# Kernel tuning notes

Hardware: AMD Instinct MI355X
Metric: run time of the kernel (lower is better)

## Reference

```python
import jax, jax.numpy as jnp
import numpy as np

# Module hyperparameters derived from init_kwargs
G = 100          # grid_size = int(n_samples ** gamma) = int(10000 ** 0.5)
K = 3            # KAN_SPLINE_ORDER
NB = G + K       # num_basis = 103
H = (1.5 - (-0.5)) / G
# grid identical for every input feature (torch expands a 1D grid)
GRID = jnp.arange(-K, G + K + 1, dtype=jnp.float32) * H - 0.5  # (G + 2K + 1,)


def bspline_basis(x):
    """Cox-de Boor recursion. x: (B, F) -> (B, F, NB)."""
    g = GRID
    xe = x[..., None]  # (B, F, 1)
    bases = ((xe >= g[:-1]) & (xe < g[1:])).astype(x.dtype)  # (B, F, G+2K)
    for k in range(1, K + 1):
        left = (xe - g[:-(k + 1)]) / jnp.maximum(g[k:-1] - g[:-(k + 1)], 1e-8)
        right = (g[k + 1:] - xe) / jnp.maximum(g[k + 1:] - g[1:-k], 1e-8)
        bases = left * bases[..., :-1] + right * bases[..., 1:]
    return bases  # (B, F, NB)


def kan_layer(x, bw, sw, wb, ws, residual):
    # base path: SiLU activation then linear
    base_out = jax.nn.silu(x) @ bw.T                      # (B, out)
    # spline path: basis expansion then contraction with spline_weight
    spline_out = jnp.einsum('bin,oin->bo', bspline_basis(x), sw)
    out = wb * base_out + ws * spline_out
    return out + x if residual else out


def setup_inputs() -> dict:
    key = jax.random.key(0)
    ks = jax.random.split(key, 16)
    B, D, W = 2048, 64, 243
    inp = {'x': jax.random.uniform(ks[0], (B, D), dtype=jnp.float32)}
    dims = [(D, W), (W, W), (W, W), (W, W), (W, W), (W, 1)]
    for i, (fi, fo) in enumerate(dims):
        kb, ksw = jax.random.split(jax.random.fold_in(key, i + 1))
        inp[f'bw{i}'] = jax.random.normal(kb, (fo, fi), dtype=jnp.float32) * (1.0 / np.sqrt(fi))
        # torch init: uniform(-0.5/G, 0.5/G)
        inp[f'sw{i}'] = jax.random.uniform(ksw, (fo, fi, NB), dtype=jnp.float32,
                                           minval=-0.5 / G, maxval=0.5 / G)
        inp[f'wb{i}'] = jnp.zeros((1,), dtype=jnp.float32)
        inp[f'ws{i}'] = jnp.ones((1,), dtype=jnp.float32)
    return inp


def reference(x, bw0, sw0, wb0, ws0, bw1, sw1, wb1, ws1, bw2, sw2, wb2, ws2,
              bw3, sw3, wb3, ws3, bw4, sw4, wb4, ws4, bw5, sw5, wb5, ws5):
    layers = [
        (bw0, sw0, wb0, ws0, False),  # 64 -> 243 (in != out: no residual)
        (bw1, sw1, wb1, ws1, True),
        (bw2, sw2, wb2, ws2, True),
        (bw3, sw3, wb3, ws3, True),
        (bw4, sw4, wb4, ws4, True),
        (bw5, sw5, wb5, ws5, False),  # 243 -> 1 (use_residual=False)
    ]
    h = x
    for bw, sw, wb, ws, res in layers:
        h = kan_layer(h, bw, sw, wb, ws, res)
    return h
```

## Files before the change

kernel.cpp:

```cpp
#include <hip/hip_runtime.h>
#include <hip/hip_fp16.h>
#include <math.h>

#define BATCH 2048
#define NBAS 103
#define NPAIR 102
#define OUTR 243
#define OUTP 256

typedef _Float16 half2v __attribute__((ext_vector_type(2)));

__device__ __forceinline__ float dot2(unsigned a, unsigned b, float c) {
#if __has_builtin(__builtin_amdgcn_fdot2)
    return __builtin_amdgcn_fdot2(__builtin_bit_cast(half2v, a),
                                  __builtin_bit_cast(half2v, b), c, false);
#else
    __half2 ha = __builtin_bit_cast(__half2, a), hb = __builtin_bit_cast(__half2, b);
    c = fmaf(__low2float(ha), __low2float(hb), c);
    c = fmaf(__high2float(ha), __high2float(hb), c);
    return c;
#endif
}

__device__ __forceinline__ uint4 make_meta(float x, int i) {
    float u = (x + 0.56f) * 50.0f;
    bool inr = (u >= 0.0f) && (u < 106.0f);
    float fj = floorf(u);
    float t = u - fj;
    int j = (int)fj;
    j = j < -1 ? -1 : (j > 106 ? 106 : j);
    float omt = 1.0f - t;
    float t2 = t * t, t3 = t2 * t;
    float w[4];
    w[0] = omt * omt * omt * (1.0f / 6.0f);
    w[1] = (3.0f * t3 - 6.0f * t2 + 4.0f) * (1.0f / 6.0f);
    w[2] = (-3.0f * t3 + 3.0f * t2 + 3.0f * t + 1.0f) * (1.0f / 6.0f);
    w[3] = t3 * (1.0f / 6.0f);
    int idx = j - 3;
    int idxc = idx < 0 ? 0 : (idx > 99 ? 99 : idx);
    int d = idx - idxc;
    float wc[4];
    #pragma unroll
    for (int m = 0; m < 4; ++m) {
        int s = m - d;
        wc[m] = (inr && s >= 0 && s < 4) ? w[s] : 0.0f;
    }
    __half2 w01 = __floats2half2_rn(wc[0], wc[1]);
    __half2 w23 = __floats2half2_rn(wc[2], wc[3]);
    uint4 m4;
    m4.x = __builtin_bit_cast(unsigned, w01);
    m4.y = __builtin_bit_cast(unsigned, w23);
    m4.z = (unsigned)((i * NPAIR + idxc) << 8);
    m4.w = (unsigned)(i * NBAS + idxc);
    return m4;
}

__device__ __forceinline__ void pairgen_body(
    const float* __restrict__ sw, int IN, unsigned* __restrict__ pairT,
    __half (*tile)[106], int i, int obase)
{
    int nl = threadIdx.x & 63;
    int w = threadIdx.x >> 6;
    #pragma unroll
    for (int k = 0; k < 8; ++k) {
        int r = w * 8 + k;
        int o = obase + r;
        if (o < OUTR) {
            const float* p = sw + ((size_t)o * IN + i) * NBAS;
            tile[r][nl] = __float2half(p[nl]);
            if (nl + 64 < NBAS)
                tile[r][nl + 64] = __float2half(p[nl + 64]);
        }
    }
    __syncthreads();
    unsigned* dst = pairT + (size_t)i * NPAIR * 256 + obase;
    for (int idx = threadIdx.x; idx < NPAIR * 32; idx += 256) {
        int p = idx >> 5, o = idx & 31;
        unsigned v = 0;
        if (obase + o < OUTR) {
            unsigned lo = __half_as_ushort(tile[o][p]);
            unsigned hi = __half_as_ushort(tile[o][p + 1]);
            v = lo | (hi << 16);
        }
        dst[(size_t)p * 256 + o] = v;
    }
}

__global__ __launch_bounds__(256) void pairgen_kernel(
    const float* __restrict__ sw, int IN, unsigned* __restrict__ pairT)
{
    __shared__ __half tile[32][106];
    pairgen_body(sw, IN, pairT, tile, blockIdx.x, blockIdx.y * 32);
}

__global__ __launch_bounds__(256) void pairgen_all_kernel(
    const float* __restrict__ sw0, const float* __restrict__ sw1,
    const float* __restrict__ sw2, const float* __restrict__ sw3,
    const float* __restrict__ sw4,
    unsigned* __restrict__ pT0, unsigned* __restrict__ pT1,
    unsigned* __restrict__ pT2, unsigned* __restrict__ pT3,
    unsigned* __restrict__ pT4,
    const float* __restrict__ xin, uint4* __restrict__ meta)
{
    __shared__ __half tile[32][106];
    int bx = blockIdx.x;
    if (bx < 512) {
        pairgen_body(sw0, 64, pT0, tile, bx >> 3, (bx & 7) * 32);
    } else if (bx < 8288) {
        int idx = bx - 512;
        int l = idx / 1944;
        int rem = idx - l * 1944;
        const float* sw; unsigned* pt;
        if (l == 0)      { sw = sw1; pt = pT1; }
        else if (l == 1) { sw = sw2; pt = pT2; }
        else if (l == 2) { sw = sw3; pt = pT3; }
        else             { sw = sw4; pt = pT4; }
        pairgen_body(sw, OUTR, pt, tile, rem >> 3, (rem & 7) * 32);
    } else {
        int e = (bx - 8288) * 256 + threadIdx.x;
        int b = e >> 6, i = e & 63;
        meta[e] = make_meta(xin[(size_t)b * 64 + i], i);
    }
}

template <int IN>
__global__ __launch_bounds__(256) void basis_kernel(
    const float* __restrict__ xin, int xstride, uint4* __restrict__ meta,
    float4* __restrict__ zbuf)
{
    int e = blockIdx.x * 256 + threadIdx.x;
    if (zbuf && e < (BATCH * OUTP) / 4) zbuf[e] = make_float4(0.f, 0.f, 0.f, 0.f);
    if (e >= BATCH * IN) return;
    int b = e / IN, i = e - b * IN;
    meta[e] = make_meta(xin[(size_t)b * xstride + i], i);
}

template <bool ADDRES>
__global__ __launch_bounds__(256) void basis_mid_kernel(
    const float* __restrict__ hprev,
    const float* __restrict__ parts,
    uint4* __restrict__ meta, float* __restrict__ hcomb)
{
    int e = blockIdx.x * 256 + threadIdx.x;
    if (e >= BATCH * OUTR) return;
    int b = e / OUTR, i = e - b * OUTR;
    size_t addr = (size_t)b * OUTP + i;
    const size_t PS = (size_t)BATCH * OUTP;
    float h = ADDRES ? hprev[addr] : 0.0f;
    #pragma unroll
    for (int s = 0; s < 8; ++s) h += parts[s * PS + addr];
    hcomb[addr] = h;
    meta[e] = make_meta(h, i);
}

template <bool ADDRES>
__global__ __launch_bounds__(256) void fused_pg_bm_kernel(
    const float* __restrict__ sw, unsigned* __restrict__ pairT,
    const float* __restrict__ hprev, const float* __restrict__ parts,
    uint4* __restrict__ meta, float* __restrict__ hcomb)
{
    if (blockIdx.y == 0) {
        __shared__ __half tile[32][106];
        pairgen_body(sw, OUTR, pairT, tile, blockIdx.x >> 3, (blockIdx.x & 7) * 32);
    } else {
        int e = blockIdx.x * 256 + threadIdx.x;
        if (e >= BATCH * OUTR) return;
        int b = e / OUTR, i = e - b * OUTR;
        size_t addr = (size_t)b * OUTP + i;
        const size_t PS = (size_t)BATCH * OUTP;
        float h = ADDRES ? hprev[addr] : 0.0f;
        #pragma unroll
        for (int s = 0; s < 8; ++s) h += parts[s * PS + addr];
        hcomb[addr] = h;
        meta[e] = make_meta(h, i);
    }
}

__global__ __launch_bounds__(256) void fused0_kernel(
    const float* __restrict__ sw0, unsigned* __restrict__ pairT,
    const float* __restrict__ xin, uint4* __restrict__ meta)
{
    if (blockIdx.y == 0) {
        __shared__ __half tile[32][106];
        pairgen_body(sw0, 64, pairT, tile, blockIdx.x >> 3, (blockIdx.x & 7) * 32);
    } else {
        int e = blockIdx.x * 256 + threadIdx.x;
        int b = e >> 6, i = e & 63;
        meta[e] = make_meta(xin[(size_t)b * 64 + i], i);
    }
}

template <int IN>
__global__ __launch_bounds__(256, 8) void layer_store_kernel(
    const unsigned* __restrict__ pairT, const uint4* __restrict__ meta,
    const float* __restrict__ h_in, int hstride,
    const float* __restrict__ bw,
    const float* __restrict__ wbp, const float* __restrict__ wsp,
    float* __restrict__ part)
{
    const int lane = threadIdx.x & 63;
    const int wave = __builtin_amdgcn_readfirstlane(threadIdx.x >> 6);
    const int b0 = blockIdx.y * 8 + wave * 2;
    const int cx = blockIdx.x;
    const int i0 = (IN * cx) >> 3;
    const int i1 = (IN * (cx + 1)) >> 3;
    const uint4* mp0 = meta + (size_t)b0 * IN;
    const uint4* mp1 = mp0 + IN;
    float a0[4] = {0.f, 0.f, 0.f, 0.f};
    float a1[4] = {0.f, 0.f, 0.f, 0.f};
    #pragma unroll 2
    for (int i = i0; i < i1; ++i) {
        uint4 m0 = mp0[i];
        uint4 m1 = mp1[i];
        const uint4* pA = (const uint4*)(pairT + m0.z) + lane;
        const uint4* pB = (const uint4*)(pairT + m1.z) + lane;
        uint4 ra = pA[0];
        uint4 rb = pA[128];
        uint4 rc = pB[0];
        uint4 rd = pB[128];
        a0[0] = dot2(m0.x, ra.x, a0[0]); a0[1] = dot2(m0.x, ra.y, a0[1]);
        a0[2] = dot2(m0.x, ra.z, a0[2]); a0[3] = dot2(m0.x, ra.w, a0[3]);
        a0[0] = dot2(m0.y, rb.x, a0[0]); a0[1] = dot2(m0.y, rb.y, a0[1]);
        a0[2] = dot2(m0.y, rb.z, a0[2]); a0[3] = dot2(m0.y, rb.w, a0[3]);
        a1[0] = dot2(m1.x, rc.x, a1[0]); a1[1] = dot2(m1.x, rc.y, a1[1]);
        a1[2] = dot2(m1.x, rc.z, a1[2]); a1[3] = dot2(m1.x, rc.w, a1[3]);
        a1[0] = dot2(m1.y, rd.x, a1[0]); a1[1] = dot2(m1.y, rd.y, a1[1]);
        a1[2] = dot2(m1.y, rd.z, a1[2]); a1[3] = dot2(m1.y, rd.w, a1[3]);
    }
    float wsv = wsp[0];
    float wbv = wbp[0];
    float4 v0 = make_float4(wsv * a0[0], wsv * a0[1], wsv * a0[2], wsv * a0[3]);
    float4 v1 = make_float4(wsv * a1[0], wsv * a1[1], wsv * a1[2], wsv * a1[3]);
    if (wbv != 0.0f) {
        float* pv0 = &v0.x; float* pv1 = &v1.x;
        for (int c = 0; c < 4; ++c) {
            int o = lane * 4 + c;
            if (o < OUTR) {
                float bs0 = 0.0f, bs1 = 0.0f;
                for (int i = i0; i < i1; ++i) {
                    float x0 = h_in[(size_t)b0 * hstride + i];
                    float x1 = h_in[(size_t)(b0 + 1) * hstride + i];
                    bs0 = fmaf(x0 / (1.0f + expf(-x0)), bw[o * IN + i], bs0);
                    bs1 = fmaf(x1 / (1.0f + expf(-x1)), bw[o * IN + i], bs1);
                }
                pv0[c] += wbv * bs0;
                pv1[c] += wbv * bs1;
            }
        }
    }
    float* d0 = part + ((size_t)cx * BATCH + b0) * OUTP + lane * 4;
    *(float4*)d0 = v0;
    *(float4*)(d0 + OUTP) = v1;
}

template <int IN, bool RES>
__global__ __launch_bounds__(256, 8) void layer_atomic_kernel(
    const unsigned* __restrict__ pairT, const uint4* __restrict__ meta,
    const float* __restrict__ h_in, int hstride,
    const float* __restrict__ bw,
    const float* __restrict__ wbp, const float* __restrict__ wsp,
    float* __restrict__ out)
{
    const int lane = threadIdx.x & 63;
    const int wave = __builtin_amdgcn_readfirstlane(threadIdx.x >> 6);
    const int b = blockIdx.y * 4 + wave;
    const int cx = blockIdx.x;
    const int i0 = (IN * cx) >> 3;
    const int i1 = (IN * (cx + 1)) >> 3;
    const uint4* mp = meta + (size_t)b * IN;
    float acc[4] = {0.f, 0.f, 0.f, 0.f};
    #pragma unroll 2
    for (int i = i0; i < i1; ++i) {
        uint4 m = mp[i];
        const uint4* pA = (const uint4*)(pairT + m.z) + lane;
        uint4 ra = pA[0];
        uint4 rb = pA[128];
        acc[0] = dot2(m.x, ra.x, acc[0]); acc[1] = dot2(m.x, ra.y, acc[1]);
        acc[2] = dot2(m.x, ra.z, acc[2]); acc[3] = dot2(m.x, ra.w, acc[3]);
        acc[0] = dot2(m.y, rb.x, acc[0]); acc[1] = dot2(m.y, rb.y, acc[1]);
        acc[2] = dot2(m.y, rb.z, acc[2]); acc[3] = dot2(m.y, rb.w, acc[3]);
    }
    float wsv = wsp[0];
    float wbv = wbp[0];
    #pragma unroll
    for (int c = 0; c < 4; ++c) {
        int o = lane * 4 + c;
        float v = wsv * acc[c];
        if (RES && cx == 0) v += h_in[(size_t)b * hstride + o];
        if (wbv != 0.0f && o < OUTR) {
            float bs = 0.0f;
            for (int i = i0; i < i1; ++i) {
                float xx = h_in[(size_t)b * hstride + i];
                bs = fmaf(xx / (1.0f + expf(-xx)), bw[o * IN + i], bs);
            }
            v += wbv * bs;
        }
        unsafeAtomicAdd(&out[(size_t)b * OUTP + o], v);
    }
}

__global__ __launch_bounds__(256) void final_fused_kernel(
    const float* __restrict__ sw5,
    const float* __restrict__ hprev,
    const float* __restrict__ parts,
    const float* __restrict__ bw5,
    const float* __restrict__ wbp, const float* __restrict__ wsp,
    float* __restrict__ out)
{
    int wave = threadIdx.x >> 6, lane = threadIdx.x & 63;
    int b = blockIdx.x * 4 + wave;
    const size_t PS = (size_t)BATCH * OUTP;
    float s = 0.0f, bs = 0.0f;
    for (int i = lane; i < OUTR; i += 64) {
        size_t addr = (size_t)b * OUTP + i;
        float h = hprev[addr];
        #pragma unroll
        for (int ss = 0; ss < 8; ++ss) h += parts[ss * PS + addr];
        uint4 m = make_meta(h, i);
        __half2 w01 = __builtin_bit_cast(__half2, m.x);
        __half2 w23 = __builtin_bit_cast(__half2, m.y);
        const float* p = sw5 + m.w;
        s += __low2float(w01) * p[0] + __high2float(w01) * p[1]
           + __low2float(w23) * p[2] + __high2float(w23) * p[3];
        bs = fmaf(h / (1.0f + expf(-h)), bw5[i], bs);
    }
    #pragma unroll
    for (int d = 32; d; d >>= 1) {
        s += __shfl_down(s, d, 64);
        bs += __shfl_down(bs, d, 64);
    }
    if (lane == 0) out[b] = wsp[0] * s + wbp[0] * bs;
}

__global__ __launch_bounds__(256) void final_kernel(
    const float* __restrict__ sw5,
    const uint4* __restrict__ meta,
    const float* __restrict__ h, const float* __restrict__ bw5,
    const float* __restrict__ wbp, const float* __restrict__ wsp,
    float* __restrict__ out)
{
    int wave = threadIdx.x >> 6, lane = threadIdx.x & 63;
    int b = blockIdx.x * 4 + wave;
    float s = 0.0f;
    for (int i = lane; i < OUTR; i += 64) {
        uint4 m = meta[(size_t)b * OUTR + i];
        __half2 w01 = __builtin_bit_cast(__half2, m.x);
        __half2 w23 = __builtin_bit_cast(__half2, m.y);
        const float* p = sw5 + m.w;
        s += __low2float(w01) * p[0] + __high2float(w01) * p[1]
           + __low2float(w23) * p[2] + __high2float(w23) * p[3];
    }
    #pragma unroll
    for (int d = 32; d; d >>= 1) s += __shfl_down(s, d, 64);
    if (lane == 0) {
        float v = wsp[0] * s;
        float wbv = wbp[0];
        if (wbv != 0.0f) {
            float bs = 0.0f;
            for (int i = 0; i < OUTR; ++i) {
                float xx = h[(size_t)b * OUTP + i];
                bs = fmaf(xx / (1.0f + expf(-xx)), bw5[i], bs);
            }
            v += wbv * bs;
        }
        out[b] = v;
    }
}

extern "C" void kernel_launch(void* const* d_in, const int* in_sizes, int n_in,
                              void* d_out, int out_size, void* d_ws, size_t ws_size,
                              hipStream_t stream)
{
    const float* x = (const float*)d_in[0];
    const float *bw[6], *sw[6], *wb[6], *ws[6];
    for (int l = 0; l < 6; ++l) {
        bw[l] = (const float*)d_in[1 + 4 * l];
        sw[l] = (const float*)d_in[2 + 4 * l];
        wb[l] = (const float*)d_in[3 + 4 * l];
        ws[l] = (const float*)d_in[4 + 4 * l];
    }
    char* base = (char*)d_ws;
    unsigned* pairT1 = (unsigned*)(base + 0);
    uint4*    meta   = (uint4*)(base + 25380864);
    float*    outp   = (float*)d_out;
    const int NB243 = (BATCH * OUTR + 255) / 256;

    const size_t NEED_ALL = 137142272;
    const size_t NEED_MID = 54315008;
    const size_t NEED_ATM = 37537792;

    if (ws_size >= NEED_ALL) {
        float*    parts  = (float*)(base + 33343488);
        float*    hcA    = (float*)(base + 50120704);
        float*    hcB    = (float*)(base + 52217856);
        unsigned* pairT0 = (unsigned*)(base + 54315008);
        unsigned* pairT2 = (unsigned*)(base + 60999680);
        unsigned* pairT3 = (unsigned*)(base + 86380544);
        unsigned* pairT4 = (unsigned*)(base + 111761408);
        unsigned* pT[5] = {pairT0, pairT1, pairT2, pairT3, pairT4};

        pairgen_all_kernel<<<8800, 256, 0, stream>>>(
            sw[0], sw[1], sw[2], sw[3], sw[4],
            pairT0, pairT1, pairT2, pairT3, pairT4, x, meta);

        layer_store_kernel<64><<<dim3(8, BATCH / 8), 256, 0, stream>>>(
            pairT0, meta, x, 64, bw[0], wb[0], ws[0], parts);

        float* hin = hcA; float* hout = hcB;
        for (int l = 1; l <= 4; ++l) {
            if (l == 1)
                basis_mid_kernel<false><<<NB243, 256, 0, stream>>>(nullptr, parts, meta, hin);
            else
                basis_mid_kernel<true><<<NB243, 256, 0, stream>>>(hout, parts, meta, hin);
            layer_store_kernel<243><<<dim3(8, BATCH / 8), 256, 0, stream>>>(
                pT[l], meta, hin, OUTP, bw[l], wb[l], ws[l], parts);
            float* tmp = hin; hin = hout; hout = tmp;
        }
        final_fused_kernel<<<BATCH / 4, 256, 0, stream>>>(
            sw[5], hout, parts, bw[5], wb[5], ws[5], outp);
    } else if (ws_size >= NEED_MID) {
        float* parts = (float*)(base + 33343488);
        float* hcA   = (float*)(base + 50120704);
        float* hcB   = (float*)(base + 52217856);

        fused0_kernel<<<dim3(512, 2), 256, 0, stream>>>(sw[0], pairT1, x, meta);
        layer_store_kernel<64><<<dim3(8, BATCH / 8), 256, 0, stream>>>(
            pairT1, meta, x, 64, bw[0], wb[0], ws[0], parts);

        float* hin = hcA; float* hout = hcB;
        for (int l = 1; l <= 4; ++l) {
            if (l == 1)
                fused_pg_bm_kernel<false><<<dim3(1944, 2), 256, 0, stream>>>(
                    sw[l], pairT1, nullptr, parts, meta, hin);
            else
                fused_pg_bm_kernel<true><<<dim3(1944, 2), 256, 0, stream>>>(
                    sw[l], pairT1, hout, parts, meta, hin);
            layer_store_kernel<243><<<dim3(8, BATCH / 8), 256, 0, stream>>>(
                pairT1, meta, hin, OUTP, bw[l], wb[l], ws[l], parts);
            float* tmp = hin; hin = hout; hout = tmp;
        }
        final_fused_kernel<<<BATCH / 4, 256, 0, stream>>>(
            sw[5], hout, parts, bw[5], wb[5], ws[5], outp);
    } else {
        if (ws_size < NEED_ATM) return;
        float* hA = (float*)(base + 33343488);
        float* hB = (float*)(base + 35440640);
        pairgen_kernel<<<dim3(64, 8), 256, 0, stream>>>(sw[0], 64, pairT1);
        basis_kernel<64><<<(BATCH * 64) / 256, 256, 0, stream>>>(x, 64, meta, (float4*)hA);
        layer_atomic_kernel<64, false><<<dim3(8, BATCH / 4), 256, 0, stream>>>(
            pairT1, meta, x, 64, bw[0], wb[0], ws[0], hA);
        float* hin = hA; float* hout = hB;
        for (int l = 1; l <= 4; ++l) {
            pairgen_kernel<<<dim3(OUTR, 8), 256, 0, stream>>>(sw[l], OUTR, pairT1);
            basis_kernel<243><<<NB243, 256, 0, stream>>>(hin, OUTP, meta, (float4*)hout);
            layer_atomic_kernel<243, true><<<dim3(8, BATCH / 4), 256, 0, stream>>>(
                pairT1, meta, hin, OUTP, bw[l], wb[l], ws[l], hout);
            float* tmp = hin; hin = hout; hout = tmp;
        }
        basis_kernel<243><<<NB243, 256, 0, stream>>>(hin, OUTP, meta, nullptr);
        final_kernel<<<BATCH / 4, 256, 0, stream>>>(sw[5], meta, hin, bw[5], wb[5], ws[5], outp);
    }
}
```

Measured before the change: 403.3 us.

## Reorganize packed spline-pair weight layout into 64-output blocks per row

Changes the pairT layout from one 256-output-wide row per basis pair to four 64-output sub-blocks per input, so that each group of 16 lanes reads a contiguous 64-output slice. The pair-generation kernels now use 64-row tiles with fewer blocks and zero-fill padded rows, and the layer kernels compute per-lane offsets for the new layout. The aim is better locality and fewer blocks in the weight repack, plus a different access pattern in the hot dot-product loop. The risk is that lanes now touch four separate 1KB segments per load instead of one contiguous span.

```diff
diff --git a/kernel.cpp b/kernel.cpp
--- a/kernel.cpp
+++ b/kernel.cpp
@@ -50,47 +50,51 @@
     uint4 m4;
     m4.x = __builtin_bit_cast(unsigned, w01);
     m4.y = __builtin_bit_cast(unsigned, w23);
-    m4.z = (unsigned)((i * NPAIR + idxc) << 8);
+    m4.z = (unsigned)((i * (NPAIR * 4) + idxc) << 6);
     m4.w = (unsigned)(i * NBAS + idxc);
     return m4;
 }
 
-__device__ __forceinline__ void pairgen_body(
+__device__ __forceinline__ void pairgen_body64(
     const float* __restrict__ sw, int IN, unsigned* __restrict__ pairT,
     __half (*tile)[106], int i, int obase)
 {
     int nl = threadIdx.x & 63;
     int w = threadIdx.x >> 6;
     #pragma unroll
-    for (int k = 0; k < 8; ++k) {
-        int r = w * 8 + k;
+    for (int k = 0; k < 16; ++k) {
+        int r = w * 16 + k;
         int o = obase + r;
         if (o < OUTR) {
             const float* p = sw + ((size_t)o * IN + i) * NBAS;
             tile[r][nl] = __float2half(p[nl]);
             if (nl + 64 < NBAS)
                 tile[r][nl + 64] = __float2half(p[nl + 64]);
+        } else {
+            tile[r][nl] = __ushort_as_half((unsigned short)0);
+            if (nl + 64 < 106)
+                tile[r][nl + 64] = __ushort_as_half((unsigned short)0);
         }
     }
     __syncthreads();
-    unsigned* dst = pairT + (size_t)i * NPAIR * 256 + obase;
-    for (int idx = threadIdx.x; idx < NPAIR * 32; idx += 256) {
-        int p = idx >> 5, o = idx & 31;
-        unsigned v = 0;
-        if (obase + o < OUTR) {
-            unsigned lo = __half_as_ushort(tile[o][p]);
-            unsigned hi = __half_as_ushort(tile[o][p + 1]);
-            v = lo | (hi << 16);
-        }
-        dst[(size_t)p * 256 + o] = v;
+    int ol = threadIdx.x & 63;
+    int rg = threadIdx.x >> 6;
+    unsigned* dst = pairT + (size_t)i * (NPAIR * 4 * 64) + (size_t)(obase >> 6) * (NPAIR * 64);
+    for (int r = 0; r < NPAIR; r += 4) {
+        int rr = r + rg;
+        if (rr < NPAIR) {
+            unsigned lo = __half_as_ushort(tile[ol][rr]);
+            unsigned hi = __half_as_ushort(tile[ol][rr + 1]);
+            dst[(size_t)rr * 64 + ol] = lo | (hi << 16);
+        }
     }
 }
 
 __global__ __launch_bounds__(256) void pairgen_kernel(
     const float* __restrict__ sw, int IN, unsigned* __restrict__ pairT)
 {
-    __shared__ __half tile[32][106];
-    pairgen_body(sw, IN, pairT, tile, blockIdx.x, blockIdx.y * 32);
+    __shared__ __half tile[64][106];
+    pairgen_body64(sw, IN, pairT, tile, blockIdx.x, blockIdx.y * 64);
 }
 
 __global__ __launch_bounds__(256) void pairgen_all_kernel(
@@ -102,22 +106,24 @@
     unsigned* __restrict__ pT4,
     const float* __restrict__ xin, uint4* __restrict__ meta)
 {
-    __shared__ __half tile[32][106];
+    __shared__ __half tile[64][106];
     int bx = blockIdx.x;
-    if (bx < 512) {
-        pairgen_body(sw0, 64, pT0, tile, bx >> 3, (bx & 7) * 32);
-    } else if (bx < 8288) {
-        int idx = bx - 512;
-        int l = idx / 1944;
-        int rem = idx - l * 1944;
-        const float* sw; unsigned* pt;
-        if (l == 0)      { sw = sw1; pt = pT1; }
-        else if (l == 1) { sw = sw2; pt = pT2; }
-        else if (l == 2) { sw = sw3; pt = pT3; }
-        else             { sw = sw4; pt = pT4; }
-        pairgen_body(sw, OUTR, pt, tile, rem >> 3, (rem & 7) * 32);
+    if (bx < 4144) {
+        const float* sw; unsigned* pt; int IN; int idx;
+        if (bx < 256) { sw = sw0; pt = pT0; IN = 64; idx = bx; }
+        else {
+            int t = bx - 256;
+            int l = t / 972;
+            idx = t - l * 972;
+            IN = OUTR;
+            if (l == 0)      { sw = sw1; pt = pT1; }
+            else if (l == 1) { sw = sw2; pt = pT2; }
+            else if (l == 2) { sw = sw3; pt = pT3; }
+            else             { sw = sw4; pt = pT4; }
+        }
+        pairgen_body64(sw, IN, pt, tile, idx >> 2, (idx & 3) * 64);
     } else {
-        int e = (bx - 8288) * 256 + threadIdx.x;
+        int e = (bx - 4144) * 256 + threadIdx.x;
         int b = e >> 6, i = e & 63;
         meta[e] = make_meta(xin[(size_t)b * 64 + i], i);
     }
@@ -160,8 +166,9 @@
     uint4* __restrict__ meta, float* __restrict__ hcomb)
 {
     if (blockIdx.y == 0) {
-        __shared__ __half tile[32][106];
-        pairgen_body(sw, OUTR, pairT, tile, blockIdx.x >> 3, (blockIdx.x & 7) * 32);
+        __shared__ __half tile[64][106];
+        if (blockIdx.x < 972)
+            pairgen_body64(sw, OUTR, pairT, tile, blockIdx.x >> 2, (blockIdx.x & 3) * 64);
     } else {
         int e = blockIdx.x * 256 + threadIdx.x;
         if (e >= BATCH * OUTR) return;
@@ -181,8 +188,9 @@
     const float* __restrict__ xin, uint4* __restrict__ meta)
 {
     if (blockIdx.y == 0) {
-        __shared__ __half tile[32][106];
-        pairgen_body(sw0, 64, pairT, tile, blockIdx.x >> 3, (blockIdx.x & 7) * 32);
+        __shared__ __half tile[64][106];
+        if (blockIdx.x < 256)
+            pairgen_body64(sw0, 64, pairT, tile, blockIdx.x >> 2, (blockIdx.x & 3) * 64);
     } else {
         int e = blockIdx.x * 256 + threadIdx.x;
         int b = e >> 6, i = e & 63;
@@ -204,6 +212,7 @@
     const int cx = blockIdx.x;
     const int i0 = (IN * cx) >> 3;
     const int i1 = (IN * (cx + 1)) >> 3;
+    const unsigned laneoff = ((unsigned)(lane >> 4) * (NPAIR * 64)) + ((unsigned)(lane & 15) << 2);
     const uint4* mp0 = meta + (size_t)b0 * IN;
     const uint4* mp1 = mp0 + IN;
     float a0[4] = {0.f, 0.f, 0.f, 0.f};
@@ -212,12 +221,12 @@
     for (int i = i0; i < i1; ++i) {
         uint4 m0 = mp0[i];
         uint4 m1 = mp1[i];
-        const uint4* pA = (const uint4*)(pairT + m0.z) + lane;
-        const uint4* pB = (const uint4*)(pairT + m1.z) + lane;
+        const uint4* pA = (const uint4*)(pairT + m0.z + laneoff);
+        const uint4* pB = (const uint4*)(pairT + m1.z + laneoff);
         uint4 ra = pA[0];
-        uint4 rb = pA[128];
+        uint4 rb = pA[32];
         uint4 rc = pB[0];
-        uint4 rd = pB[128];
+        uint4 rd = pB[32];
         a0[0] = dot2(m0.x, ra.x, a0[0]); a0[1] = dot2(m0.x, ra.y, a0[1]);
         a0[2] = dot2(m0.x, ra.z, a0[2]); a0[3] = dot2(m0.x, ra.w, a0[3]);
         a0[0] = dot2(m0.y, rb.x, a0[0]); a0[1] = dot2(m0.y, rb.y, a0[1]);
@@ -267,14 +276,15 @@
     const int cx = blockIdx.x;
     const int i0 = (IN * cx) >> 3;
     const int i1 = (IN * (cx + 1)) >> 3;
+    const unsigned laneoff = ((unsigned)(lane >> 4) * (NPAIR * 64)) + ((unsigned)(lane & 15) << 2);
     const uint4* mp = meta + (size_t)b * IN;
     float acc[4] = {0.f, 0.f, 0.f, 0.f};
     #pragma unroll 2
     for (int i = i0; i < i1; ++i) {
         uint4 m = mp[i];
-        const uint4* pA = (const uint4*)(pairT + m.z) + lane;
+        const uint4* pA = (const uint4*)(pairT + m.z + laneoff);
         uint4 ra = pA[0];
-        uint4 rb = pA[128];
+        uint4 rb = pA[32];
         acc[0] = dot2(m.x, ra.x, acc[0]); acc[1] = dot2(m.x, ra.y, acc[1]);
         acc[2] = dot2(m.x, ra.z, acc[2]); acc[3] = dot2(m.x, ra.w, acc[3]);
         acc[0] = dot2(m.y, rb.x, acc[0]); acc[1] = dot2(m.y, rb.y, acc[1]);
@@ -399,7 +409,7 @@
         unsigned* pairT4 = (unsigned*)(base + 111761408);
         unsigned* pT[5] = {pairT0, pairT1, pairT2, pairT3, pairT4};
 
-        pairgen_all_kernel<<<8800, 256, 0, stream>>>(
+        pairgen_all_kernel<<<4656, 256, 0, stream>>>(
             sw[0], sw[1], sw[2], sw[3], sw[4],
             pairT0, pairT1, pairT2, pairT3, pairT4, x, meta);
 
@@ -445,13 +455,13 @@
         if (ws_size < NEED_ATM) return;
         float* hA = (float*)(base + 33343488);
         float* hB = (float*)(base + 35440640);
-        pairgen_kernel<<<dim3(64, 8), 256, 0, stream>>>(sw[0], 64, pairT1);
+        pairgen_kernel<<<dim3(64, 4), 256, 0, stream>>>(sw[0], 64, pairT1);
         basis_kernel<64><<<(BATCH * 64) / 256, 256, 0, stream>>>(x, 64, meta, (float4*)hA);
         layer_atomic_kernel<64, false><<<dim3(8, BATCH / 4), 256, 0, stream>>>(
             pairT1, meta, x, 64, bw[0], wb[0], ws[0], hA);
         float* hin = hA; float* hout = hB;
         for (int l = 1; l <= 4; ++l) {
-            pairgen_kernel<<<dim3(OUTR, 8), 256, 0, stream>>>(sw[l], OUTR, pairT1);
+            pairgen_kernel<<<dim3(OUTR, 4), 256, 0, stream>>>(sw[l], OUTR, pairT1);
             basis_kernel<243><<<NB243, 256, 0, stream>>>(hin, OUTP, meta, (float4*)hout);
             layer_atomic_kernel<243, true><<<dim3(8, BATCH / 4), 256, 0, stream>>>(
                 pairT1, meta, hin, OUTP, bw[l], wb[l], ws[l], hout);
```

New measurement: 412.9 us. +2.4%, slower.

## Generate per-layer spline pair tables lazily and manually unroll the basis loop

Applied to the files above, without the earlier changes.

The up-front kernel that converted all five layers' spline weights into fp16 pair tables is replaced. A smaller front kernel now builds only the layer 0 and layer 1 tables plus the input metadata. Layers 2-4 reuse a single pairT buffer, and each table is built by the fused pairgen+basis kernel just before that layer runs. This needs a smaller workspace and gives better cache locality, but conversion work is now serialized between layers. Separately, the inner dot-product loop is manually unrolled by two so the table loads for two input features are issued before the math.

```diff
diff --git a/kernel.cpp b/kernel.cpp
--- a/kernel.cpp
+++ b/kernel.cpp
@@ -93,31 +93,22 @@
     pairgen_body(sw, IN, pairT, tile, blockIdx.x, blockIdx.y * 32);
 }
 
-__global__ __launch_bounds__(256) void pairgen_all_kernel(
-    const float* __restrict__ sw0, const float* __restrict__ sw1,
-    const float* __restrict__ sw2, const float* __restrict__ sw3,
-    const float* __restrict__ sw4,
-    unsigned* __restrict__ pT0, unsigned* __restrict__ pT1,
-    unsigned* __restrict__ pT2, unsigned* __restrict__ pT3,
-    unsigned* __restrict__ pT4,
+__global__ __launch_bounds__(256) void front_kernel(
+    const float* __restrict__ sw0, unsigned* __restrict__ pT0,
+    const float* __restrict__ sw1, unsigned* __restrict__ pT1,
     const float* __restrict__ xin, uint4* __restrict__ meta)
 {
-    __shared__ __half tile[32][106];
     int bx = blockIdx.x;
-    if (bx < 512) {
-        pairgen_body(sw0, 64, pT0, tile, bx >> 3, (bx & 7) * 32);
-    } else if (bx < 8288) {
-        int idx = bx - 512;
-        int l = idx / 1944;
-        int rem = idx - l * 1944;
-        const float* sw; unsigned* pt;
-        if (l == 0)      { sw = sw1; pt = pT1; }
-        else if (l == 1) { sw = sw2; pt = pT2; }
-        else if (l == 2) { sw = sw3; pt = pT3; }
-        else             { sw = sw4; pt = pT4; }
-        pairgen_body(sw, OUTR, pt, tile, rem >> 3, (rem & 7) * 32);
+    if (bx < 2456) {
+        __shared__ __half tile[32][106];
+        if (bx < 512)
+            pairgen_body(sw0, 64, pT0, tile, bx >> 3, (bx & 7) * 32);
+        else {
+            int t = bx - 512;
+            pairgen_body(sw1, OUTR, pT1, tile, t >> 3, (t & 7) * 32);
+        }
     } else {
-        int e = (bx - 8288) * 256 + threadIdx.x;
+        int e = (bx - 2456) * 256 + threadIdx.x;
         int b = e >> 6, i = e & 63;
         meta[e] = make_meta(xin[(size_t)b * 64 + i], i);
     }
@@ -208,8 +199,42 @@
     const uint4* mp1 = mp0 + IN;
     float a0[4] = {0.f, 0.f, 0.f, 0.f};
     float a1[4] = {0.f, 0.f, 0.f, 0.f};
-    #pragma unroll 2
-    for (int i = i0; i < i1; ++i) {
+    int i = i0;
+    for (; i + 1 < i1; i += 2) {
+        uint4 m0 = mp0[i];
+        uint4 m1 = mp1[i];
+        uint4 n0 = mp0[i + 1];
+        uint4 n1 = mp1[i + 1];
+        const uint4* pA = (const uint4*)(pairT + m0.z) + lane;
+        const uint4* pB = (const uint4*)(pairT + m1.z) + lane;
+        const uint4* qA = (const uint4*)(pairT + n0.z) + lane;
+        const uint4* qB = (const uint4*)(pairT + n1.z) + lane;
+        uint4 ra = pA[0];
+        uint4 rb = pA[128];
+        uint4 rc = pB[0];
+        uint4 rd = pB[128];
+        uint4 sa = qA[0];
+        uint4 sb = qA[128];
+        uint4 sc = qB[0];
+        uint4 sd = qB[128];
+        a0[0] = dot2(m0.x, ra.x, a0[0]); a0[1] = dot2(m0.x, ra.y, a0[1]);
+        a0[2] = dot2(m0.x, ra.z, a0[2]); a0[3] = dot2(m0.x, ra.w, a0[3]);
+        a0[0] = dot2(m0.y, rb.x, a0[0]); a0[1] = dot2(m0.y, rb.y, a0[1]);
+        a0[2] = dot2(m0.y, rb.z, a0[2]); a0[3] = dot2(m0.y, rb.w, a0[3]);
+        a1[0] = dot2(m1.x, rc.x, a1[0]); a1[1] = dot2(m1.x, rc.y, a1[1]);
+        a1[2] = dot2(m1.x, rc.z, a1[2]); a1[3] = dot2(m1.x, rc.w, a1[3]);
+        a1[0] = dot2(m1.y, rd.x, a1[0]); a1[1] = dot2(m1.y, rd.y, a1[1]);
+        a1[2] = dot2(m1.y, rd.z, a1[2]); a1[3] = dot2(m1.y, rd.w, a1[3]);
+        a0[0] = dot2(n0.x, sa.x, a0[0]); a0[1] = dot2(n0.x, sa.y, a0[1]);
+        a0[2] = dot2(n0.x, sa.z, a0[2]); a0[3] = dot2(n0.x, sa.w, a0[3]);
+        a0[0] = dot2(n0.y, sb.x, a0[0]); a0[1] = dot2(n0.y, sb.y, a0[1]);
+        a0[2] = dot2(n0.y, sb.z, a0[2]); a0[3] = dot2(n0.y, sb.w, a0[3]);
+        a1[0] = dot2(n1.x, sc.x, a1[0]); a1[1] = dot2(n1.x, sc.y, a1[1]);
+        a1[2] = dot2(n1.x, sc.z, a1[2]); a1[3] = dot2(n1.x, sc.w, a1[3]);
+        a1[0] = dot2(n1.y, sd.x, a1[0]); a1[1] = dot2(n1.y, sd.y, a1[1]);
+        a1[2] = dot2(n1.y, sd.z, a1[2]); a1[3] = dot2(n1.y, sd.w, a1[3]);
+    }
+    if (i < i1) {
         uint4 m0 = mp0[i];
         uint4 m1 = mp1[i];
         const uint4* pA = (const uint4*)(pairT + m0.z) + lane;
@@ -237,11 +262,11 @@
             int o = lane * 4 + c;
             if (o < OUTR) {
                 float bs0 = 0.0f, bs1 = 0.0f;
-                for (int i = i0; i < i1; ++i) {
-                    float x0 = h_in[(size_t)b0 * hstride + i];
-                    float x1 = h_in[(size_t)(b0 + 1) * hstride + i];
-                    bs0 = fmaf(x0 / (1.0f + expf(-x0)), bw[o * IN + i], bs0);
-                    bs1 = fmaf(x1 / (1.0f + expf(-x1)), bw[o * IN + i], bs1);
+                for (int k = i0; k < i1; ++k) {
+                    float x0 = h_in[(size_t)b0 * hstride + k];
+                    float x1 = h_in[(size_t)(b0 + 1) * hstride + k];
+                    bs0 = fmaf(x0 / (1.0f + expf(-x0)), bw[o * IN + k], bs0);
+                    bs1 = fmaf(x1 / (1.0f + expf(-x1)), bw[o * IN + k], bs1);
                 }
                 pv0[c] += wbv * bs0;
                 pv1[c] += wbv * bs1;
@@ -380,40 +405,36 @@
         ws[l] = (const float*)d_in[4 + 4 * l];
     }
     char* base = (char*)d_ws;
+    float* outp = (float*)d_out;
+    const int NB243 = (BATCH * OUTR + 255) / 256;
+
+    const size_t NEED_FRONT = 60999680;
+    const size_t NEED_MID = 54315008;
+    const size_t NEED_ATM = 37537792;
+
     unsigned* pairT1 = (unsigned*)(base + 0);
     uint4*    meta   = (uint4*)(base + 25380864);
-    float*    outp   = (float*)d_out;
-    const int NB243 = (BATCH * OUTR + 255) / 256;
-
-    const size_t NEED_ALL = 137142272;
-    const size_t NEED_MID = 54315008;
-    const size_t NEED_ATM = 37537792;
-
-    if (ws_size >= NEED_ALL) {
-        float*    parts  = (float*)(base + 33343488);
-        float*    hcA    = (float*)(base + 50120704);
-        float*    hcB    = (float*)(base + 52217856);
-        unsigned* pairT0 = (unsigned*)(base + 54315008);
-        unsigned* pairT2 = (unsigned*)(base + 60999680);
-        unsigned* pairT3 = (unsigned*)(base + 86380544);
-        unsigned* pairT4 = (unsigned*)(base + 111761408);
-        unsigned* pT[5] = {pairT0, pairT1, pairT2, pairT3, pairT4};
-
-        pairgen_all_kernel<<<8800, 256, 0, stream>>>(
-            sw[0], sw[1], sw[2], sw[3], sw[4],
-            pairT0, pairT1, pairT2, pairT3, pairT4, x, meta);
+
+    if (ws_size >= NEED_FRONT) {
+        float*    parts = (float*)(base + 33343488);
+        float*    hcA   = (float*)(base + 50120704);
+        float*    hcB   = (float*)(base + 52217856);
+        unsigned* T0    = (unsigned*)(base + 54315008);
+
+        front_kernel<<<2968, 256, 0, stream>>>(sw[0], T0, sw[1], pairT1, x, meta);
 
         layer_store_kernel<64><<<dim3(8, BATCH / 8), 256, 0, stream>>>(
-            pairT0, meta, x, 64, bw[0], wb[0], ws[0], parts);
+            T0, meta, x, 64, bw[0], wb[0], ws[0], parts);
 
         float* hin = hcA; float* hout = hcB;
         for (int l = 1; l <= 4; ++l) {
             if (l == 1)
                 basis_mid_kernel<false><<<NB243, 256, 0, stream>>>(nullptr, parts, meta, hin);
             else
-                basis_mid_kernel<true><<<NB243, 256, 0, stream>>>(hout, parts, meta, hin);
+                fused_pg_bm_kernel<true><<<dim3(1944, 2), 256, 0, stream>>>(
+                    sw[l], pairT1, hout, parts, meta, hin);
             layer_store_kernel<243><<<dim3(8, BATCH / 8), 256, 0, stream>>>(
-                pT[l], meta, hin, OUTP, bw[l], wb[l], ws[l], parts);
+                pairT1, meta, hin, OUTP, bw[l], wb[l], ws[l], parts);
             float* tmp = hin; hin = hout; hout = tmp;
         }
         final_fused_kernel<<<BATCH / 4, 256, 0, stream>>>(
```

Measured after the change: 398.3 us. About the same (-1.2%).
